# Performance work log

Hardware: AMD Instinct MI355X
Metric: run time of the kernel (lower is better)

Reference implementation:

```python
import jax, jax.numpy as jnp
import numpy as np

B, S, T = 512, 1024, 64

def setup_inputs() -> dict:
    key = jax.random.key(0)
    k1, k2, k3 = jax.random.split(key, 3)
    feats = jax.random.normal(k1, (B, S, T), dtype=jnp.float32)
    tags = jax.random.randint(k2, (B, S), 0, T, dtype=jnp.int64)
    mask = jnp.ones((B, S), dtype=jnp.bool_)
    trans_m = jax.random.normal(k3, (T, T), dtype=jnp.float32)
    return {"feats": feats, "tags": tags, "mask": mask, "trans_m": trans_m}

def _crf_nll(feats, tags, mask, trans_m):
    # to time-major: [S, B, T], [S, B]
    logits = jnp.transpose(feats, (1, 0, 2))
    tags_t = jnp.transpose(tags, (1, 0))
    mask_t = jnp.transpose(mask, (1, 0))

    # ---- normalizer (forward algorithm) ----
    alpha0 = logits[0]  # [B, T]

    def step(alpha, inp):
        emit, m = inp  # emit: [B, T], m: [B] bool
        # tmp[b, i, j] = alpha[b, i] + emit[b, j] + trans_m[i, j]
        tmp = alpha[:, :, None] + emit[:, None, :] + trans_m[None, :, :]
        lse = jax.nn.logsumexp(tmp, axis=1)  # [B, T]
        alpha_new = jnp.where(m[:, None], lse, alpha)
        return alpha_new, None

    alpha, _ = jax.lax.scan(step, alpha0, (logits[1:], mask_t[1:]))
    norm = jax.nn.logsumexp(alpha, axis=1)  # [B]

    # ---- gold path score ----
    emit = jnp.take_along_axis(logits, tags_t[:, :, None], axis=2)[:, :, 0]  # [S, B]
    emit = jnp.where(mask_t, emit, 0.0)
    trans = trans_m[tags_t[:-1], tags_t[1:]]  # [S-1, B]
    trans = jnp.where(mask_t[1:], trans, 0.0)
    gold = emit.sum(axis=0) + trans.sum(axis=0)  # [B]

    return norm - gold

def reference(feats, tags, mask, trans_m):
    return _crf_nll(feats, tags, mask, trans_m)
```

## Files before the change

### kernel.cpp

```cpp
#include <hip/hip_runtime.h>
#include <cstdint>
#include <cstddef>


#define S_ 1024
#define T_ 64

typedef float f32x2 __attribute__((ext_vector_type(2)));
typedef float f32x4 __attribute__((ext_vector_type(4)));

__device__ __forceinline__ float rl_f(float v, int lane) {
  return __int_as_float(__builtin_amdgcn_readlane(__float_as_int(v), lane));
}

template <int CTRL>
__device__ __forceinline__ float dppq(float v) {
  return __int_as_float(__builtin_amdgcn_update_dpp(
      0, __float_as_int(v), CTRL, 0xF, 0xF, true));
}

#define FMA4(AVX, AVY, P) { \
  f32x2 av_; av_.x = (AVX); av_.y = (AVY); \
  P0_ += av_ * er2[0][P]; P1_ += av_ * er2[1][P]; \
  P2_ += av_ * er2[2][P]; P3_ += av_ * er2[3][P]; }

#define BPF(K) __int_as_float(__builtin_amdgcn_ds_bpermute(bidx##K, aw_))

#define STEPF(TMT, ECU, EEU) { \
  const int tmt_ = (TMT); \
  const int tag_ = tmt_ & 255; \
  const int mk_  = (tmt_ >> 8) & 1; \
  const float ce_ = (EEU) * scale_pend; \
  const int aw_ = __float_as_int(Aprev); \
  const float b0_  = BPF(0),  b1_  = BPF(1),  b2_  = BPF(2),  b3_  = BPF(3); \
  const float b4_  = BPF(4),  b5_  = BPF(5),  b6_  = BPF(6),  b7_  = BPF(7); \
  const float b8_  = BPF(8),  b9_  = BPF(9),  b10_ = BPF(10), b11_ = BPF(11); \
  const float b12_ = BPF(12), b13_ = BPF(13), b14_ = BPF(14), b15_ = BPF(15); \
  f32x2 P0_ = {0.f, 0.f}, P1_ = {0.f, 0.f}, P2_ = {0.f, 0.f}, P3_ = {0.f, 0.f}; \
  FMA4(b0_,  b1_,  0); FMA4(b2_,  b3_,  1); \
  FMA4(b4_,  b5_,  2); FMA4(b6_,  b7_,  3); \
  FMA4(b8_,  b9_,  4); FMA4(b10_, b11_, 5); \
  FMA4(b12_, b13_, 6); FMA4(b14_, b15_, 7); \
  float p0_ = P0_.x + P0_.y, p1_ = P1_.x + P1_.y; \
  float p2_ = P2_.x + P2_.y, p3_ = P3_.x + P3_.y; \
  float qq0_ = p0_ + dppq<0xB1>(p0_); \
  float qq1_ = p1_ + dppq<0xB1>(p1_); \
  float qq2_ = p2_ + dppq<0xB1>(p2_); \
  float qq3_ = p3_ + dppq<0xB1>(p3_); \
  float r0_ = qq0_ + dppq<0x4E>(qq0_); \
  float r1_ = qq1_ + dppq<0x4E>(qq1_); \
  float r2_ = qq2_ + dppq<0x4E>(qq2_); \
  float r3_ = qq3_ + dppq<0x4E>(qq3_); \
  float s01_ = (c & 1) ? r1_ : r0_; \
  float s23_ = (c & 1) ? r3_ : r2_; \
  float s_ = (c & 2) ? s23_ : s01_; \
  float An_ = s_ * ce_; \
  Aprev = mk_ ? An_ : Aprev; \
  Mk += mk_ ? pend : 0; \
  int wb_ = __builtin_amdgcn_readfirstlane(__float_as_int(Aprev)); \
  pend = (int)(((unsigned)wb_ >> 23) & 255) - 127; \
  scale_pend = __int_as_float((127 - pend) << 23); \
  gold += mk_ ? rl_f((ECU), tag_) : 0.0f; \
}

#define RL(V, U) __builtin_amdgcn_readlane((V), (U))

__launch_bounds__(64)
__attribute__((amdgpu_waves_per_eu(1, 1)))
__global__ void crf_scan(const float* __restrict__ feats,
                         const int* __restrict__ tags,
                         const int* __restrict__ mask,
                         const float* __restrict__ trans,
                         float* __restrict__ out) {
  const int b = blockIdx.x;
  const int lane = threadIdx.x;
  const int g = lane >> 2;
  const int c = lane & 3;

  __shared__ int tmeta[S_];

  const float LOG2E = 1.4426950408889634f;

  const int bidx0  = (16 * c + 0)  << 2, bidx1  = (16 * c + 1)  << 2;
  const int bidx2  = (16 * c + 2)  << 2, bidx3  = (16 * c + 3)  << 2;
  const int bidx4  = (16 * c + 4)  << 2, bidx5  = (16 * c + 5)  << 2;
  const int bidx6  = (16 * c + 6)  << 2, bidx7  = (16 * c + 7)  << 2;
  const int bidx8  = (16 * c + 8)  << 2, bidx9  = (16 * c + 9)  << 2;
  const int bidx10 = (16 * c + 10) << 2, bidx11 = (16 * c + 11) << 2;
  const int bidx12 = (16 * c + 12) << 2, bidx13 = (16 * c + 13) << 2;
  const int bidx14 = (16 * c + 14) << 2, bidx15 = (16 * c + 15) << 2;

  const int* tagb = tags + (size_t)b * S_;
  const int* mb = mask + (size_t)b * S_;
  #pragma unroll
  for (int t0 = 0; t0 < S_; t0 += 64) {
    int t = t0 + lane;
    tmeta[t] = (tagb[t] & 63) | (mb[t] != 0 ? 256 : 0);
  }

  f32x2 er2[4][8];
  #pragma unroll
  for (int r = 0; r < 4; ++r) {
    #pragma unroll
    for (int p = 0; p < 8; ++p) {
      int i0 = 16 * c + 2 * p;
      int j = 4 * g + r;
      f32x2 e;
      e.x = exp2f(trans[(size_t)i0 * T_ + j] * LOG2E);
      e.y = exp2f(trans[(size_t)(i0 + 1) * T_ + j] * LOG2E);
      er2[r][p] = e;
    }
  }

  float gtr = 0.0f;
  #pragma unroll
  for (int u = 0; u < 16; ++u) {
    int t = lane * 16 + u + 1;
    if (t < S_) {
      int m1 = tmeta[t];
      if (m1 & 256) {
        int m0 = tmeta[t - 1];
        gtr += trans[(m0 & 255) * T_ + (m1 & 255)];
      }
    }
  }

  const float* fb = feats + (size_t)b * S_ * T_ + lane;
  float e0i = fb[0];
  float Aprev = exp2f(e0i * LOG2E);
  int Mk = 0;
  int wb0 = __builtin_amdgcn_readfirstlane(__float_as_int(Aprev));
  int pend = (int)(((unsigned)wb0 >> 23) & 255) - 127;
  float scale_pend = __int_as_float((127 - pend) << 23);

  int tm0 = __builtin_amdgcn_readfirstlane(tmeta[0]);
  float gold = (tm0 & 256) ? rl_f(e0i, tm0 & 255) : 0.0f;

  float epf0 = fb[(size_t)1 * T_], epf1 = fb[(size_t)2 * T_];
  float epf2 = fb[(size_t)3 * T_], epf3 = fb[(size_t)4 * T_];
  float epf4 = fb[(size_t)5 * T_], epf5 = fb[(size_t)6 * T_];
  float epf6 = fb[(size_t)7 * T_], epf7 = fb[(size_t)8 * T_];

  for (int cc = 0; cc < 127; ++cc) {
    const int tbase = 1 + cc * 8;

    float ec0 = epf0, ec1 = epf1, ec2 = epf2, ec3 = epf3;
    float ec4 = epf4, ec5 = epf5, ec6 = epf6, ec7 = epf7;
    float ex0 = exp2f(ec0 * LOG2E), ex1 = exp2f(ec1 * LOG2E);
    float ex2 = exp2f(ec2 * LOG2E), ex3 = exp2f(ec3 * LOG2E);
    float ex4 = exp2f(ec4 * LOG2E), ex5 = exp2f(ec5 * LOG2E);
    float ex6 = exp2f(ec6 * LOG2E), ex7 = exp2f(ec7 * LOG2E);

    int tmv = tmeta[tbase + (lane & 7)];

    {
      const float* fpn = fb + (size_t)(tbase + 8) * T_;
      epf0 = fpn[0 * T_]; epf1 = fpn[1 * T_];
      epf2 = fpn[2 * T_]; epf3 = fpn[3 * T_];
      epf4 = fpn[4 * T_]; epf5 = fpn[5 * T_];
      epf6 = fpn[6 * T_];
      int t7 = tbase + 15;
      epf7 = fb[(size_t)(t7 < S_ ? t7 : S_ - 1) * T_];
    }

    STEPF(RL(tmv, 0), ec0, ex0);
    STEPF(RL(tmv, 1), ec1, ex1);
    STEPF(RL(tmv, 2), ec2, ex2);
    STEPF(RL(tmv, 3), ec3, ex3);
    STEPF(RL(tmv, 4), ec4, ex4);
    STEPF(RL(tmv, 5), ec5, ex5);
    STEPF(RL(tmv, 6), ec6, ex6);
    STEPF(RL(tmv, 7), ec7, ex7);
  }

  {
    int tt = 1017 + (lane & 7);
    if (tt > 1023) tt = 1023;
    int tmv = tmeta[tt];
    float ex0 = exp2f(epf0 * LOG2E), ex1 = exp2f(epf1 * LOG2E);
    float ex2 = exp2f(epf2 * LOG2E), ex3 = exp2f(epf3 * LOG2E);
    float ex4 = exp2f(epf4 * LOG2E), ex5 = exp2f(epf5 * LOG2E);
    float ex6 = exp2f(epf6 * LOG2E);

    STEPF(RL(tmv, 0), epf0, ex0);
    STEPF(RL(tmv, 1), epf1, ex1);
    STEPF(RL(tmv, 2), epf2, ex2);
    STEPF(RL(tmv, 3), epf3, ex3);
    STEPF(RL(tmv, 4), epf4, ex4);
    STEPF(RL(tmv, 5), epf5, ex5);
    STEPF(RL(tmv, 6), epf6, ex6);
  }

  float ssum = Aprev;
  float gsum = gtr;
  #pragma unroll
  for (int k = 32; k >= 1; k >>= 1) {
    ssum += __shfl_xor(ssum, k, 64);
    gsum += __shfl_xor(gsum, k, 64);
  }
  double norm = ((double)Mk + (double)log2f(ssum)) * 0.6931471805599453;
  double goldall = (double)gold + (double)gsum;
  if (lane == 0) out[b] = (float)(norm - goldall);
}

extern "C" void kernel_launch(void* const* d_in, const int* in_sizes, int n_in,
                              void* d_out, int out_size, void* d_ws, size_t ws_size,
                              hipStream_t stream) {
  const float* feats = (const float*)d_in[0];
  const int* tags = (const int*)d_in[1];
  const int* mask = (const int*)d_in[2];
  const float* trans = (const float*)d_in[3];
  float* out = (float*)d_out;

  int Bn = in_sizes[0] / (S_ * T_);
  hipLaunchKernelGGL(crf_scan, dim3(Bn), dim3(64), 0, stream,
                     feats, tags, mask, trans, out);
}
```

Baseline: 407.5 us.

## Replace bpermute gather with DPP row-rotate broadcast and swizzle-based reduction

Restructures the per-step matrix-vector product so each lane reads the 16 alpha values of its own row through DPP row_ror instead of 16 LDS bpermute gathers. Each lane now computes partial sums for four output columns spaced 16 apart, and these are combined across the four 16-lane rows with one ds_swizzle and two bpermutes. The transition matrix is preloaded in the matching rotated layout. This moves most of the cross-lane traffic off the LDS pipeline onto DPP operands, in exchange for extra selects and a layout that is harder to follow.

```diff
diff --git a/kernel.cpp b/kernel.cpp
--- a/kernel.cpp
+++ b/kernel.cpp
@@ -7,53 +7,48 @@
 #define T_ 64
 
 typedef float f32x2 __attribute__((ext_vector_type(2)));
-typedef float f32x4 __attribute__((ext_vector_type(4)));
 
 __device__ __forceinline__ float rl_f(float v, int lane) {
   return __int_as_float(__builtin_amdgcn_readlane(__float_as_int(v), lane));
 }
 
-template <int CTRL>
-__device__ __forceinline__ float dppq(float v) {
-  return __int_as_float(__builtin_amdgcn_update_dpp(
-      0, __float_as_int(v), CTRL, 0xF, 0xF, true));
-}
-
-#define FMA4(AVX, AVY, P) { \
-  f32x2 av_; av_.x = (AVX); av_.y = (AVY); \
-  P0_ += av_ * er2[0][P]; P1_ += av_ * er2[1][P]; \
-  P2_ += av_ * er2[2][P]; P3_ += av_ * er2[3][P]; }
-
-#define BPF(K) __int_as_float(__builtin_amdgcn_ds_bpermute(bidx##K, aw_))
+#define RORF(K) __int_as_float(__builtin_amdgcn_update_dpp( \
+    0, __float_as_int(Aprev), 0x120 + (K), 0xF, 0xF, true))
+
+#define SWZ16(X) __int_as_float(__builtin_amdgcn_ds_swizzle(__float_as_int(X), 0x401F))
+#define BPERMF(IDX, X) __int_as_float(__builtin_amdgcn_ds_bpermute((IDX), __float_as_int(X)))
+
+#define FMA4R(AV, K2) { \
+  P0_ += (AV) * er2[0][K2]; P1_ += (AV) * er2[1][K2]; \
+  P2_ += (AV) * er2[2][K2]; P3_ += (AV) * er2[3][K2]; }
 
 #define STEPF(TMT, ECU, EEU) { \
   const int tmt_ = (TMT); \
   const int tag_ = tmt_ & 255; \
   const int mk_  = (tmt_ >> 8) & 1; \
   const float ce_ = (EEU) * scale_pend; \
-  const int aw_ = __float_as_int(Aprev); \
-  const float b0_  = BPF(0),  b1_  = BPF(1),  b2_  = BPF(2),  b3_  = BPF(3); \
-  const float b4_  = BPF(4),  b5_  = BPF(5),  b6_  = BPF(6),  b7_  = BPF(7); \
-  const float b8_  = BPF(8),  b9_  = BPF(9),  b10_ = BPF(10), b11_ = BPF(11); \
-  const float b12_ = BPF(12), b13_ = BPF(13), b14_ = BPF(14), b15_ = BPF(15); \
+  f32x2 av0_, av1_, av2_, av3_, av4_, av5_, av6_, av7_; \
+  av0_.x = Aprev;    av0_.y = RORF(1); \
+  av1_.x = RORF(2);  av1_.y = RORF(3); \
+  av2_.x = RORF(4);  av2_.y = RORF(5); \
+  av3_.x = RORF(6);  av3_.y = RORF(7); \
+  av4_.x = RORF(8);  av4_.y = RORF(9); \
+  av5_.x = RORF(10); av5_.y = RORF(11); \
+  av6_.x = RORF(12); av6_.y = RORF(13); \
+  av7_.x = RORF(14); av7_.y = RORF(15); \
   f32x2 P0_ = {0.f, 0.f}, P1_ = {0.f, 0.f}, P2_ = {0.f, 0.f}, P3_ = {0.f, 0.f}; \
-  FMA4(b0_,  b1_,  0); FMA4(b2_,  b3_,  1); \
-  FMA4(b4_,  b5_,  2); FMA4(b6_,  b7_,  3); \
-  FMA4(b8_,  b9_,  4); FMA4(b10_, b11_, 5); \
-  FMA4(b12_, b13_, 6); FMA4(b14_, b15_, 7); \
+  FMA4R(av0_, 0); FMA4R(av1_, 1); FMA4R(av2_, 2); FMA4R(av3_, 3); \
+  FMA4R(av4_, 4); FMA4R(av5_, 5); FMA4R(av6_, 6); FMA4R(av7_, 7); \
   float p0_ = P0_.x + P0_.y, p1_ = P1_.x + P1_.y; \
   float p2_ = P2_.x + P2_.y, p3_ = P3_.x + P3_.y; \
-  float qq0_ = p0_ + dppq<0xB1>(p0_); \
-  float qq1_ = p1_ + dppq<0xB1>(p1_); \
-  float qq2_ = p2_ + dppq<0xB1>(p2_); \
-  float qq3_ = p3_ + dppq<0xB1>(p3_); \
-  float r0_ = qq0_ + dppq<0x4E>(qq0_); \
-  float r1_ = qq1_ + dppq<0x4E>(qq1_); \
-  float r2_ = qq2_ + dppq<0x4E>(qq2_); \
-  float r3_ = qq3_ + dppq<0x4E>(qq3_); \
-  float s01_ = (c & 1) ? r1_ : r0_; \
-  float s23_ = (c & 1) ? r3_ : r2_; \
-  float s_ = (c & 2) ? s23_ : s01_; \
+  float e0_ = is16 ? (is32 ? p3_ : p1_) : (is32 ? p2_ : p0_);   \
+  float e1_ = is16 ? (is32 ? p2_ : p0_) : (is32 ? p3_ : p1_);   \
+  float e2_ = is16 ? (is32 ? p1_ : p3_) : (is32 ? p0_ : p2_);   \
+  float e3_ = is16 ? (is32 ? p0_ : p2_) : (is32 ? p1_ : p3_);   \
+  float n1_ = SWZ16(e1_); \
+  float n2_ = BPERMF(bp32i, e2_); \
+  float n3_ = BPERMF(bp48i, e3_); \
+  float s_ = (e0_ + n1_) + (n2_ + n3_); \
   float An_ = s_ * ce_; \
   Aprev = mk_ ? An_ : Aprev; \
   Mk += mk_ ? pend : 0; \
@@ -74,21 +69,15 @@
                          float* __restrict__ out) {
   const int b = blockIdx.x;
   const int lane = threadIdx.x;
-  const int g = lane >> 2;
-  const int c = lane & 3;
+  const int p = lane & 15;
+  const bool is16 = (lane & 16) != 0;
+  const bool is32 = (lane & 32) != 0;
+  const int bp32i = (lane ^ 32) << 2;
+  const int bp48i = (lane ^ 48) << 2;
 
   __shared__ int tmeta[S_];
 
   const float LOG2E = 1.4426950408889634f;
-
-  const int bidx0  = (16 * c + 0)  << 2, bidx1  = (16 * c + 1)  << 2;
-  const int bidx2  = (16 * c + 2)  << 2, bidx3  = (16 * c + 3)  << 2;
-  const int bidx4  = (16 * c + 4)  << 2, bidx5  = (16 * c + 5)  << 2;
-  const int bidx6  = (16 * c + 6)  << 2, bidx7  = (16 * c + 7)  << 2;
-  const int bidx8  = (16 * c + 8)  << 2, bidx9  = (16 * c + 9)  << 2;
-  const int bidx10 = (16 * c + 10) << 2, bidx11 = (16 * c + 11) << 2;
-  const int bidx12 = (16 * c + 12) << 2, bidx13 = (16 * c + 13) << 2;
-  const int bidx14 = (16 * c + 14) << 2, bidx15 = (16 * c + 15) << 2;
 
   const int* tagb = tags + (size_t)b * S_;
   const int* mb = mask + (size_t)b * S_;
@@ -98,17 +87,34 @@
     tmeta[t] = (tagb[t] & 63) | (mb[t] != 0 ? 256 : 0);
   }
 
+  const int idx0 = lane;
+  const int idx1  = __builtin_amdgcn_update_dpp(0, lane, 0x121, 0xF, 0xF, true);
+  const int idx2  = __builtin_amdgcn_update_dpp(0, lane, 0x122, 0xF, 0xF, true);
+  const int idx3  = __builtin_amdgcn_update_dpp(0, lane, 0x123, 0xF, 0xF, true);
+  const int idx4  = __builtin_amdgcn_update_dpp(0, lane, 0x124, 0xF, 0xF, true);
+  const int idx5  = __builtin_amdgcn_update_dpp(0, lane, 0x125, 0xF, 0xF, true);
+  const int idx6  = __builtin_amdgcn_update_dpp(0, lane, 0x126, 0xF, 0xF, true);
+  const int idx7  = __builtin_amdgcn_update_dpp(0, lane, 0x127, 0xF, 0xF, true);
+  const int idx8  = __builtin_amdgcn_update_dpp(0, lane, 0x128, 0xF, 0xF, true);
+  const int idx9  = __builtin_amdgcn_update_dpp(0, lane, 0x129, 0xF, 0xF, true);
+  const int idx10 = __builtin_amdgcn_update_dpp(0, lane, 0x12A, 0xF, 0xF, true);
+  const int idx11 = __builtin_amdgcn_update_dpp(0, lane, 0x12B, 0xF, 0xF, true);
+  const int idx12 = __builtin_amdgcn_update_dpp(0, lane, 0x12C, 0xF, 0xF, true);
+  const int idx13 = __builtin_amdgcn_update_dpp(0, lane, 0x12D, 0xF, 0xF, true);
+  const int idx14 = __builtin_amdgcn_update_dpp(0, lane, 0x12E, 0xF, 0xF, true);
+  const int idx15 = __builtin_amdgcn_update_dpp(0, lane, 0x12F, 0xF, 0xF, true);
+  const int idxs[16] = {idx0, idx1, idx2, idx3, idx4, idx5, idx6, idx7,
+                        idx8, idx9, idx10, idx11, idx12, idx13, idx14, idx15};
+
   f32x2 er2[4][8];
   #pragma unroll
-  for (int r = 0; r < 4; ++r) {
+  for (int m = 0; m < 4; ++m) {
     #pragma unroll
-    for (int p = 0; p < 8; ++p) {
-      int i0 = 16 * c + 2 * p;
-      int j = 4 * g + r;
+    for (int k2 = 0; k2 < 8; ++k2) {
       f32x2 e;
-      e.x = exp2f(trans[(size_t)i0 * T_ + j] * LOG2E);
-      e.y = exp2f(trans[(size_t)(i0 + 1) * T_ + j] * LOG2E);
-      er2[r][p] = e;
+      e.x = exp2f(trans[(size_t)idxs[2 * k2]     * T_ + 16 * m + p] * LOG2E);
+      e.y = exp2f(trans[(size_t)idxs[2 * k2 + 1] * T_ + 16 * m + p] * LOG2E);
+      er2[m][k2] = e;
     }
   }
 
```

After: 391.6 us. 3.9% less time.
